# Performance work log

Hardware: AMD Instinct MI355X
Metric: run time of the kernel (lower is better)

Reference implementation:

```python
import jax, jax.numpy as jnp
import numpy as np

EMBED_DIM = 1024
NUM_HEADS = 16
HEAD_DIM = EMBED_DIM // NUM_HEADS
FF_DIM = 4096
B, T, S = 2, 2048, 2048
LN_EPS = 1e-5


def setup_inputs() -> dict:
    key = jax.random.key(0)
    ks = jax.random.split(key, 20)
    sd = 1.0 / np.sqrt(EMBED_DIM)
    d = {
        'x': jax.random.normal(ks[0], (B, T, EMBED_DIM), jnp.float32),
        'encoder_outputs': jax.random.normal(ks[1], (B, S, EMBED_DIM), jnp.float32),
        'tgt_mask': jnp.tril(jnp.ones((T, T), bool))[None, None],  # [1,1,T,T] causal
    }
    # weights stored [in, out] so y = x @ W + b
    names = ['sa_wq', 'sa_wk', 'sa_wv', 'sa_wo', 'ca_wq', 'ca_wk', 'ca_wv', 'ca_wo']
    for i, n in enumerate(names):
        d[n] = jax.random.normal(ks[2 + i], (EMBED_DIM, EMBED_DIM), jnp.float32) * sd
        d[n.replace('w', 'b')] = jnp.zeros((EMBED_DIM,), jnp.float32)
    d['ff_w1'] = jax.random.normal(ks[10], (EMBED_DIM, FF_DIM), jnp.float32) * sd
    d['ff_b1'] = jnp.zeros((FF_DIM,), jnp.float32)
    d['ff_w2'] = jax.random.normal(ks[11], (FF_DIM, EMBED_DIM), jnp.float32) * (1.0 / np.sqrt(FF_DIM))
    d['ff_b2'] = jnp.zeros((EMBED_DIM,), jnp.float32)
    for i in (1, 2, 3):
        d[f'ln{i}_g'] = jnp.ones((EMBED_DIM,), jnp.float32)
        d[f'ln{i}_b'] = jnp.zeros((EMBED_DIM,), jnp.float32)
    return d


def _layernorm(x, g, b):
    mu = jnp.mean(x, -1, keepdims=True)
    var = jnp.mean(jnp.square(x - mu), -1, keepdims=True)
    return (x - mu) * jax.lax.rsqrt(var + LN_EPS) * g + b


def _mha(q_in, k_in, v_in, wq, bq, wk, bk, wv, bv, wo, bo, mask=None):
    Bq, Tq, C = q_in.shape
    Tk = k_in.shape[1]
    Q = (q_in @ wq + bq).reshape(Bq, Tq, NUM_HEADS, HEAD_DIM)
    K = (k_in @ wk + bk).reshape(Bq, Tk, NUM_HEADS, HEAD_DIM)
    V = (v_in @ wv + bv).reshape(Bq, Tk, NUM_HEADS, HEAD_DIM)
    scores = jnp.einsum('bqhd,bkhd->bhqk', Q, K) / np.sqrt(HEAD_DIM)
    if mask is not None:
        scores = jnp.where(mask, scores, -jnp.inf)
    attn = jax.nn.softmax(scores, axis=-1)
    out = jnp.einsum('bhqk,bkhd->bqhd', attn, V).reshape(Bq, Tq, C)
    return out @ wo + bo


def reference(x, encoder_outputs, tgt_mask,
              sa_wq, sa_bq, sa_wk, sa_bk, sa_wv, sa_bv, sa_wo, sa_bo,
              ca_wq, ca_bq, ca_wk, ca_bk, ca_wv, ca_bv, ca_wo, ca_bo,
              ff_w1, ff_b1, ff_w2, ff_b2,
              ln1_g, ln1_b, ln2_g, ln2_b, ln3_g, ln3_b):
    h = _layernorm(x, ln1_g, ln1_b)
    x = x + _mha(h, h, h, sa_wq, sa_bq, sa_wk, sa_bk, sa_wv, sa_bv, sa_wo, sa_bo, tgt_mask)
    h = _layernorm(x, ln2_g, ln2_b)
    x = x + _mha(h, encoder_outputs, encoder_outputs,
                 ca_wq, ca_bq, ca_wk, ca_bk, ca_wv, ca_bv, ca_wo, ca_bo, None)
    h = _layernorm(x, ln3_g, ln3_b)
    ff = jax.nn.relu(h @ ff_w1 + ff_b1) @ ff_w2 + ff_b2
    return x + ff
```

## Files before the change

### kernel.cpp

```cpp
#include <hip/hip_runtime.h>
#include <stdint.h>


typedef __bf16 bf16x8 __attribute__((ext_vector_type(8)));
typedef float  f32x4  __attribute__((ext_vector_type(4)));

#define T_SEQ 2048
#define NROWS 4096
#define QSCALE 0.18033688011112042f

__device__ __forceinline__ unsigned short f2bf(float f) {
  union { float f; unsigned int u; } v; v.f = f;
  unsigned int u = v.u;
  return (unsigned short)((u + 0x7FFFu + ((u >> 16) & 1u)) >> 16);
}
__device__ __forceinline__ float bf2f(unsigned short h) {
  union { unsigned int u; float f; } v; v.u = ((unsigned int)h) << 16;
  return v.f;
}
__device__ __forceinline__ unsigned int pk2(float a, float b) {
  return (unsigned int)f2bf(a) | ((unsigned int)f2bf(b) << 16);
}
__device__ __forceinline__ unsigned int pk2t(float a, float b) {
  union { float f; unsigned int u; } ua, ub;
  ua.f = a; ub.f = b;
  return __builtin_amdgcn_perm(ub.u, ua.u, 0x07060302u);
}
__device__ __forceinline__ float fexp2(float x) {
  return __builtin_amdgcn_exp2f(x);
}
union U4 { unsigned int u[4]; bf16x8 v; };

__global__ void probe_dtype_kernel(const unsigned short* __restrict__ p,
                                   int* __restrict__ flag) {
  __shared__ int cnt;
  if (threadIdx.x == 0) cnt = 0;
  __syncthreads();
  int bad = 0;
  for (int i = threadIdx.x; i < 4096; i += 256) {
    unsigned short u = p[i];
    int e = (u >> 7) & 0xFF;
    if (u != 0 && (e < 100 || e > 140)) bad++;
  }
  atomicAdd(&cnt, bad);
  __syncthreads();
  if (threadIdx.x == 0) *flag = (cnt < 512) ? 1 : 0;
}

struct WTbl {
  const void* src[10];
  int K[10], N[10], start[10];
  unsigned int dstoff[10];
};
__global__ void wtrans_fused_kernel(WTbl tbl, unsigned short* __restrict__ wsbase,
                                    const int* __restrict__ flag) {
  __shared__ unsigned short tile[32][33];
  const int lb = blockIdx.x;
  int wi = 0;
#pragma unroll
  for (int i = 1; i < 10; i++) wi = (lb >= tbl.start[i]) ? i : wi;
  const int local = lb - tbl.start[wi];
  const int Nw = tbl.N[wi], Kw = tbl.K[wi];
  const int bx = local & ((Nw >> 5) - 1);
  const int by = local / (Nw >> 5);
  const void* W = tbl.src[wi];
  unsigned short* Wt = wsbase + tbl.dstoff[wi];
  const int n0 = bx * 32, k0 = by * 32;
  const int c = threadIdx.x & 31, r0 = threadIdx.x >> 5;
  const bool isbf = (*flag != 0);
  for (int r = r0; r < 32; r += 8) {
    unsigned short v;
    if (isbf) v = ((const unsigned short*)W)[(size_t)(k0 + r) * Nw + n0 + c];
    else      v = f2bf(((const float*)W)[(size_t)(k0 + r) * Nw + n0 + c]);
    tile[r][c] = v;
  }
  __syncthreads();
  for (int r = r0; r < 32; r += 8)
    Wt[(size_t)(n0 + r) * Kw + k0 + c] = tile[c][r];
}

struct PTbl { const void* p[19]; };
__global__ void param_cvt_kernel(PTbl tbl, float* __restrict__ out,
                                 const int* __restrict__ flag) {
  const int blk = blockIdx.x;
  const int off = (blk >= 8 && blk < 12) ? (blk - 8) * 1024 : 0;
  const void* src = tbl.p[blk];
  const int i = threadIdx.x * 4;
  float4 o;
  if (*flag) {
    const unsigned short* u = (const unsigned short*)src + off;
    ushort4 q = *(const ushort4*)&u[i];
    o.x = bf2f(q.x); o.y = bf2f(q.y); o.z = bf2f(q.z); o.w = bf2f(q.w);
  } else {
    o = *(const float4*)&((const float*)src)[off + i];
  }
  *(float4*)&out[blk * 1024 + i] = o;
}

__global__ void cvt_to_bf16_kernel(const void* __restrict__ in,
                                   unsigned short* __restrict__ out,
                                   int n, const int* __restrict__ flag) {
  int i = (blockIdx.x * 256 + threadIdx.x) * 8;
  if (i >= n) return;
  if (*flag) {
    *(int4*)&out[i] = *(const int4*)&((const unsigned short*)in)[i];
  } else {
    const float* f = (const float*)in;
    float4 a = *(const float4*)&f[i];
    float4 c = *(const float4*)&f[i + 4];
    ushort4 o1, o2;
    o1.x = f2bf(a.x); o1.y = f2bf(a.y); o1.z = f2bf(a.z); o1.w = f2bf(a.w);
    o2.x = f2bf(c.x); o2.y = f2bf(c.y); o2.z = f2bf(c.z); o2.w = f2bf(c.w);
    *(ushort4*)&out[i] = o1;
    *(ushort4*)&out[i + 4] = o2;
  }
}

__global__ void cvt_to_f32_kernel(const void* __restrict__ in,
                                  float* __restrict__ out,
                                  int n, const int* __restrict__ flag) {
  int i = (blockIdx.x * 256 + threadIdx.x) * 4;
  if (i >= n) return;
  if (*flag) {
    const unsigned short* u = (const unsigned short*)in;
    ushort4 q = *(const ushort4*)&u[i];
    float4 o;
    o.x = bf2f(q.x); o.y = bf2f(q.y); o.z = bf2f(q.z); o.w = bf2f(q.w);
    *(float4*)&out[i] = o;
  } else {
    *(float4*)&out[i] = *(const float4*)&((const float*)in)[i];
  }
}

__global__ __launch_bounds__(256) void ln_kernel(
    const float* __restrict__ x, const float* __restrict__ g,
    const float* __restrict__ b, unsigned short* __restrict__ out) {
  const int row = blockIdx.x;
  const int t = threadIdx.x;
  const size_t base = (size_t)row * 1024;
  float4 v = *(const float4*)&x[base + t * 4];
  float s1 = v.x + v.y + v.z + v.w;
  float s2 = v.x * v.x + v.y * v.y + v.z * v.z + v.w * v.w;
#pragma unroll
  for (int d = 1; d < 64; d <<= 1) {
    s1 += __shfl_xor(s1, d, 64);
    s2 += __shfl_xor(s2, d, 64);
  }
  __shared__ float a1[4], a2[4];
  if ((t & 63) == 0) { a1[t >> 6] = s1; a2[t >> 6] = s2; }
  __syncthreads();
  s1 = a1[0] + a1[1] + a1[2] + a1[3];
  s2 = a2[0] + a2[1] + a2[2] + a2[3];
  const float mean = s1 * (1.0f / 1024.0f);
  const float var = s2 * (1.0f / 1024.0f) - mean * mean;
  const float rstd = rsqrtf(fmaxf(var, 0.0f) + 1e-5f);
  float4 gv = *(const float4*)&g[t * 4];
  float4 bv = *(const float4*)&b[t * 4];
  ushort4 o;
  o.x = f2bf((v.x - mean) * rstd * gv.x + bv.x);
  o.y = f2bf((v.y - mean) * rstd * gv.y + bv.y);
  o.z = f2bf((v.z - mean) * rstd * gv.z + bv.z);
  o.w = f2bf((v.w - mean) * rstd * gv.w + bv.w);
  *(ushort4*)&out[base + t * 4] = o;
}

template <int BM, int BN, int BK, int RELU, int RESID, int OUTM, int BIASROW,
          int SCALEMODE>
__global__ __launch_bounds__(256, 2) void gemm_kernel(
    const unsigned short* __restrict__ A, const unsigned short* __restrict__ Bt,
    const float* __restrict__ bias, const float* __restrict__ resid,
    void* __restrict__ outp, int M, int N, int K,
    const int* __restrict__ flag) {
  static_assert(BK == 64, "swizzle assumes 8 chunks/row");
  constexpr int WX = (BN == 64) ? 1 : 2;
  constexpr int WY = 4 / WX;
  constexpr int WM = BM / WY, WN = BN / WX;
  constexpr int MI = WM / 16, NJ = WN / 16;
  constexpr int ACALLS = BM * BK / 2048;
  constexpr int BCALLS = BN * BK / 2048;
  constexpr int RPC = 2048 / BK;
  __shared__ unsigned short lsA[2][BM * BK];
  __shared__ unsigned short lsB[2][BN * BK];
  const int t = threadIdx.x;
  const int wave = t >> 6, lane = t & 63;
  const int ml = lane & 15, quad = lane >> 4;
  const int cx = ml & 7;
  const int wm = (wave / WX) * WM, wn = (wave % WX) * WN;

  const int nx = gridDim.x, ny = gridDim.y;
  const int lin = (int)blockIdx.y * nx + (int)blockIdx.x;
  const int per = 8 * nx;
  const int y0 = (lin / per) * 8;
  const int gsz = (ny - y0 < 8) ? (ny - y0) : 8;
  const int by = y0 + (lin % gsz);
  const int bx = (lin % per) / gsz;
  const size_t m0 = (size_t)by * BM;
  const size_t n0 = (size_t)bx * BN;

  f32x4 acc[MI][NJ];
  const f32x4 fz = {0.f, 0.f, 0.f, 0.f};
#pragma unroll
  for (int i = 0; i < MI; i++)
#pragma unroll
    for (int j = 0; j < NJ; j++) acc[i][j] = fz;

  const int rowL = t >> 3;
  const int colL = (((t & 7) ^ ((t >> 3) & 7)) * 8);
  const unsigned short* gA = A + (m0 + rowL) * (size_t)K + colL;
  const unsigned short* gB = Bt + (n0 + rowL) * (size_t)K + colL;

  auto stage = [&](int buf, int k0) {
#pragma unroll
    for (int c = 0; c < ACALLS; c++)
      __builtin_amdgcn_global_load_lds(
          (const __attribute__((address_space(1))) void*)(gA + (size_t)(c * RPC) * K + k0),
          (__attribute__((address_space(3))) void*)&lsA[buf][c * 2048 + wave * 512], 16, 0, 0);
#pragma unroll
    for (int c = 0; c < BCALLS; c++)
      __builtin_amdgcn_global_load_lds(
          (const __attribute__((address_space(1))) void*)(gB + (size_t)(c * RPC) * K + k0),
          (__attribute__((address_space(3))) void*)&lsB[buf][c * 2048 + wave * 512], 16, 0, 0);
  };

  stage(0, 0);
  const int nk = K / BK;
  for (int tk = 0; tk < nk; ++tk) {
    const int cur = tk & 1;
    asm volatile("s_waitcnt vmcnt(0)" ::: "memory");
    __builtin_amdgcn_s_barrier();
    if (tk + 1 < nk) stage(cur ^ 1, (tk + 1) * BK);
#pragma unroll
    for (int h = 0; h < BK / 32; h++) {
      bf16x8 af[MI], bfv[NJ];
#pragma unroll
      for (int i = 0; i < MI; i++)
        af[i] = *(const bf16x8*)
            &lsA[cur][(wm + i * 16 + ml) * BK + (((h * 4 + quad) ^ cx) * 8)];
#pragma unroll
      for (int j = 0; j < NJ; j++)
        bfv[j] = *(const bf16x8*)
            &lsB[cur][(wn + j * 16 + ml) * BK + (((h * 4 + quad) ^ cx) * 8)];
#pragma unroll
      for (int i = 0; i < MI; i++)
#pragma unroll
        for (int j = 0; j < NJ; j++)
          acc[i][j] = __builtin_amdgcn_mfma_f32_16x16x32_bf16(af[i], bfv[j],
                                                              acc[i][j], 0, 0, 0);
    }
  }

  const bool obf = (OUTM == 1) || (OUTM == 2 && *flag != 0);
#pragma unroll
  for (int j = 0; j < NJ; j++) {
    const size_t cg = n0 + wn + j * 16 + ml;
    const float bcol = BIASROW ? 0.0f : bias[cg];
    const float sc = (SCALEMODE == 0) ? 1.0f
                   : (SCALEMODE == 1) ? QSCALE
                                      : (cg < 1024 ? QSCALE : 1.0f);
#pragma unroll
    for (int i = 0; i < MI; i++) {
#pragma unroll
      for (int r = 0; r < 4; r++) {
        const size_t rg = m0 + wm + i * 16 + quad * 4 + r;
        const float bval = BIASROW ? bias[rg] : bcol;
        float v = (acc[i][j][r] + bval) * sc;
        if (RELU) v = fmaxf(v, 0.0f);
        if (RESID) v += resid[rg * N + cg];
        if (obf) ((unsigned short*)outp)[rg * N + cg] = f2bf(v);
        else     ((float*)outp)[rg * N + cg] = v;
      }
    }
  }
}

struct GSeg {
  const unsigned short* A; const unsigned short* B;
  const float* bias; unsigned short* out;
  int N, K, start, gxlog2, mode;
};
template <int NSEG>
__global__ __launch_bounds__(256, 4) void gemm_multi_kernel(GSeg s0, GSeg s1,
                                                            GSeg s2) {
  constexpr int BM = 128, BN = 64, BK = 64;
  constexpr int WM = 32, WN = 64;
  constexpr int MI = 2, NJ = 4;
  __shared__ unsigned short lsA[BM * BK];
  __shared__ unsigned short lsB[BN * BK];
  const int blk = (int)blockIdx.x;
  GSeg sg = s0;
  if (NSEG > 1 && blk >= s1.start) sg = s1;
  if (NSEG > 2 && blk >= s2.start) sg = s2;
  const int t = threadIdx.x;
  const int wave = t >> 6, lane = t & 63;
  const int ml = lane & 15, quad = lane >> 4;
  const int cx = ml & 7;
  const int wm = wave * WM, wn = 0;
  const int N = sg.N, K = sg.K;

  const int lin = blk - sg.start;
  const int per = 8 << sg.gxlog2;
  const int y0 = (lin / per) * 8;
  const int by = y0 + (lin & 7);
  const int bx = (lin & (per - 1)) >> 3;
  const size_t m0 = (size_t)by * BM;
  const size_t n0 = (size_t)bx * BN;

  f32x4 acc[MI][NJ];
  const f32x4 fz = {0.f, 0.f, 0.f, 0.f};
#pragma unroll
  for (int i = 0; i < MI; i++)
#pragma unroll
    for (int j = 0; j < NJ; j++) acc[i][j] = fz;

  const int rowL = t >> 3;
  const int colL = (((t & 7) ^ ((t >> 3) & 7)) * 8);
  const unsigned short* gA = sg.A + (m0 + rowL) * (size_t)K + colL;
  const unsigned short* gB = sg.B + (n0 + rowL) * (size_t)K + colL;

  for (int k0 = 0; k0 < K; k0 += BK) {
    __syncthreads();
#pragma unroll
    for (int c = 0; c < 4; c++)
      __builtin_amdgcn_global_load_lds(
          (const __attribute__((address_space(1))) void*)(gA + (size_t)(c * 32) * K + k0),
          (__attribute__((address_space(3))) void*)&lsA[c * 2048 + wave * 512], 16, 0, 0);
#pragma unroll
    for (int c = 0; c < 2; c++)
      __builtin_amdgcn_global_load_lds(
          (const __attribute__((address_space(1))) void*)(gB + (size_t)(c * 32) * K + k0),
          (__attribute__((address_space(3))) void*)&lsB[c * 2048 + wave * 512], 16, 0, 0);
    __syncthreads();
#pragma unroll
    for (int h = 0; h < BK / 32; h++) {
      bf16x8 af[MI], bfv[NJ];
#pragma unroll
      for (int i = 0; i < MI; i++)
        af[i] = *(const bf16x8*)
            &lsA[(wm + i * 16 + ml) * BK + (((h * 4 + quad) ^ cx) * 8)];
#pragma unroll
      for (int j = 0; j < NJ; j++)
        bfv[j] = *(const bf16x8*)
            &lsB[(wn + j * 16 + ml) * BK + (((h * 4 + quad) ^ cx) * 8)];
#pragma unroll
      for (int i = 0; i < MI; i++)
#pragma unroll
        for (int j = 0; j < NJ; j++)
          acc[i][j] = __builtin_amdgcn_mfma_f32_16x16x32_bf16(af[i], bfv[j],
                                                              acc[i][j], 0, 0, 0);
    }
  }

  const int mode = sg.mode;
#pragma unroll
  for (int j = 0; j < NJ; j++) {
    const size_t cg = n0 + wn + j * 16 + ml;
    const float bcol = (mode & 1) ? 0.0f : sg.bias[cg];
    const float sc = (mode & 2) ? QSCALE
                   : ((mode & 4) && cg < 1024) ? QSCALE : 1.0f;
#pragma unroll
    for (int i = 0; i < MI; i++) {
#pragma unroll
      for (int r = 0; r < 4; r++) {
        const size_t rg = m0 + wm + i * 16 + quad * 4 + r;
        const float bval = (mode & 1) ? sg.bias[rg] : bcol;
        float v = (acc[i][j][r] + bval) * sc;
        sg.out[rg * N + cg] = f2bf(v);
      }
    }
  }
}

template <int CAUSAL>
__global__ __launch_bounds__(256, 4) void attn_kernel(
    const unsigned short* __restrict__ Q, const unsigned short* __restrict__ K,
    const unsigned short* __restrict__ VT, unsigned short* __restrict__ O,
    int qstride, int kstride) {
  __shared__ unsigned short Ks[4096];
  __shared__ unsigned short Vs[4096];
  __shared__ unsigned short Qs[4608];
  const int t = threadIdx.x;
  const int wave = t >> 6, lane = t & 63;
  const int ml = lane & 15, quad = lane >> 4;
  const int cx = ml & 7;
  const int bh = blockIdx.y, b = bh >> 4, h = bh & 15;
  const int qb = CAUSAL ? ((int)gridDim.x - 1 - (int)blockIdx.x) : (int)blockIdx.x;
  const int q0 = qb * 64;
  const int lr = lane >> 3;
  const int scol = (((lane & 7) ^ lr) * 8);

  {
    const unsigned short* g0 =
        Q + ((size_t)(b * T_SEQ + q0 + wave * 16 + lr)) * qstride + h * 64 + scol;
    __builtin_amdgcn_global_load_lds(
        (const __attribute__((address_space(1))) void*)g0,
        (__attribute__((address_space(3))) void*)&Qs[wave * 2 * 512], 16, 0, 0);
    const unsigned short* g1 = g0 + (size_t)8 * qstride;
    __builtin_amdgcn_global_load_lds(
        (const __attribute__((address_space(1))) void*)g1,
        (__attribute__((address_space(3))) void*)&Qs[(wave * 2 + 1) * 512], 16, 0, 0);
  }

  int sp_[2];
#pragma unroll
  for (int i = 0; i < 2; i++) {
    int p = (wave * 2 + i) * 8 + lr;
    sp_[i] = ((p & 16) << 1) | ((p & 12) << 1) | ((p & 32) >> 3) | (p & 3);
  }
  const unsigned short* kg0 =
      K + ((size_t)b * T_SEQ + sp_[0]) * kstride + h * 64 + scol;
  const unsigned short* kg1 =
      K + ((size_t)b * T_SEQ + sp_[1]) * kstride + h * 64 + scol;
  const unsigned short* vg0 =
      VT + ((size_t)(h * 64 + wave * 16 + lr)) * 4096 + (size_t)b * T_SEQ + scol;
  const unsigned short* vg1 = vg0 + (size_t)8 * 4096;

  __syncthreads();
  const bf16x8 aq0 = *(const bf16x8*)&Qs[(wave * 16 + ml) * 64 + ((quad ^ cx) * 8)];
  const bf16x8 aq1 = *(const bf16x8*)&Qs[(wave * 16 + ml) * 64 + (((quad + 4) ^ cx) * 8)];

  f32x4 acc[4];
  const f32x4 fz = {0.f, 0.f, 0.f, 0.f};
#pragma unroll
  for (int n = 0; n < 4; n++) acc[n] = fz;
  float m_i = -3.0e38f, l_part = 0.0f;
  const int q_glob = q0 + wave * 16 + ml;
  const int nkb = CAUSAL ? (qb + 1) : (T_SEQ / 64);
  const size_t kinc = (size_t)64 * kstride;

  for (int kb = 0; kb < nkb; kb++) {
    __syncthreads();
    __builtin_amdgcn_global_load_lds(
        (const __attribute__((address_space(1))) void*)kg0,
        (__attribute__((address_space(3))) void*)&Ks[(wave * 2) * 512], 16, 0, 0);
    __builtin_amdgcn_global_load_lds(
        (const __attribute__((address_space(1))) void*)kg1,
        (__attribute__((address_space(3))) void*)&Ks[(wave * 2 + 1) * 512], 16, 0, 0);
    __builtin_amdgcn_global_load_lds(
        (const __attribute__((address_space(1))) void*)vg0,
        (__attribute__((address_space(3))) void*)&Vs[(wave * 2) * 512], 16, 0, 0);
    __builtin_amdgcn_global_load_lds(
        (const __attribute__((address_space(1))) void*)vg1,
        (__attribute__((address_space(3))) void*)&Vs[(wave * 2 + 1) * 512], 16, 0, 0);
    kg0 += kinc; kg1 += kinc; vg0 += 64; vg1 += 64;
    __syncthreads();

    f32x4 s[4];
#pragma unroll
    for (int nt = 0; nt < 4; nt++) {
      bf16x8 k0 = *(const bf16x8*)&Ks[(nt * 16 + ml) * 64 + ((quad ^ cx) * 8)];
      bf16x8 k1 = *(const bf16x8*)&Ks[(nt * 16 + ml) * 64 + (((quad + 4) ^ cx) * 8)];
      f32x4 a = fz;
      a = __builtin_amdgcn_mfma_f32_16x16x32_bf16(k0, aq0, a, 0, 0, 0);
      a = __builtin_amdgcn_mfma_f32_16x16x32_bf16(k1, aq1, a, 0, 0, 0);
      s[nt] = a;
    }
    if (CAUSAL && kb == nkb - 1) {
#pragma unroll
      for (int nt = 0; nt < 4; nt++)
#pragma unroll
        for (int r = 0; r < 4; r++) {
          int key = kb * 64 + ((nt & 1) << 5) + (quad << 3) + ((nt >> 1) << 2) + r;
          if (key > q_glob) s[nt][r] = -3.0e38f;
        }
    }
    float tm = -3.0e38f;
#pragma unroll
    for (int nt = 0; nt < 4; nt++)
#pragma unroll
      for (int r = 0; r < 4; r++) tm = fmaxf(tm, s[nt][r]);
    tm = fmaxf(tm, __shfl_xor(tm, 16));
    tm = fmaxf(tm, __shfl_xor(tm, 32));
    if (__any(tm > m_i)) {
      const float m_new = fmaxf(m_i, tm);
      const float alpha = fexp2(m_i - m_new);
      l_part *= alpha;
#pragma unroll
      for (int n = 0; n < 4; n++)
#pragma unroll
        for (int r = 0; r < 4; r++) acc[n][r] *= alpha;
      m_i = m_new;
    }
    float p[4][4];
    float rs = 0.f;
#pragma unroll
    for (int nt = 0; nt < 4; nt++)
#pragma unroll
      for (int r = 0; r < 4; r++) {
        p[nt][r] = fexp2(s[nt][r] - m_i);
        rs += p[nt][r];
      }
    l_part += rs;

    U4 P0, P1;
    P0.u[0] = pk2t(p[0][0], p[0][1]); P0.u[1] = pk2t(p[0][2], p[0][3]);
    P0.u[2] = pk2t(p[2][0], p[2][1]); P0.u[3] = pk2t(p[2][2], p[2][3]);
    P1.u[0] = pk2t(p[1][0], p[1][1]); P1.u[1] = pk2t(p[1][2], p[1][3]);
    P1.u[2] = pk2t(p[3][0], p[3][1]); P1.u[3] = pk2t(p[3][2], p[3][3]);

#pragma unroll
    for (int n = 0; n < 4; n++) {
      bf16x8 v0 = *(const bf16x8*)&Vs[(n * 16 + ml) * 64 + ((quad ^ cx) * 8)];
      bf16x8 v1 = *(const bf16x8*)&Vs[(n * 16 + ml) * 64 + (((quad + 4) ^ cx) * 8)];
      acc[n] = __builtin_amdgcn_mfma_f32_16x16x32_bf16(v0, P0.v, acc[n], 0, 0, 0);
      acc[n] = __builtin_amdgcn_mfma_f32_16x16x32_bf16(v1, P1.v, acc[n], 0, 0, 0);
    }
  }

  float l_i = l_part;
  l_i += __shfl_xor(l_i, 16);
  l_i += __shfl_xor(l_i, 32);

  const float inv = 1.0f / l_i;
#pragma unroll
  for (int n = 0; n < 4; n++)
#pragma unroll
    for (int rp = 0; rp < 2; rp++) {
      unsigned int u = pk2(acc[n][2 * rp] * inv, acc[n][2 * rp + 1] * inv);
      *(unsigned int*)&Qs[(wave * 16 + ml) * 72 + n * 16 + quad * 4 + 2 * rp] = u;
    }
  __syncthreads();
  {
    const int q = t >> 2, d0 = (t & 3) * 16;
    unsigned short* og = O + ((size_t)(b * T_SEQ + q0 + q)) * 1024 + h * 64 + d0;
    *(int4*)og = *(const int4*)&Qs[q * 72 + d0];
    *(int4*)(og + 8) = *(const int4*)&Qs[q * 72 + d0 + 8];
  }
}

extern "C" void kernel_launch(void* const* d_in, const int* in_sizes, int n_in,
                              void* d_out, int out_size, void* d_ws,
                              size_t ws_size, hipStream_t stream) {
  (void)in_sizes; (void)n_in; (void)out_size; (void)ws_size;
  const size_t MEG = 1048576;
  unsigned short* ws16 = (unsigned short*)d_ws;
  char* wsb = (char*)d_ws;

  unsigned short* wt[10];
  for (int i = 0; i < 8; i++) wt[i] = ws16 + (size_t)i * MEG;
  wt[8] = ws16 + 8 * MEG;
  wt[9] = ws16 + 12 * MEG;
  unsigned short* encB  = ws16 + 16 * MEG;
  unsigned short* hbuf  = ws16 + 20 * MEG;
  unsigned short* QKb   = ws16 + 24 * MEG;
  unsigned short* Qb    = ws16 + 32 * MEG;
  unsigned short* Kb    = ws16 + 36 * MEG;
  unsigned short* Vb    = ws16 + 40 * MEG;
  unsigned short* attnb = ws16 + 44 * MEG;
  unsigned short* ffh   = ws16 + 24 * MEG;
  float* xf32 = (float*)(wsb + 96 * MEG);
  float* pbuf = (float*)(wsb + 112 * MEG);
  int* flag   = (int*)(wsb + 113 * MEG);

  probe_dtype_kernel<<<1, 256, 0, stream>>>((const unsigned short*)d_in[0], flag);

  {
    WTbl tb;
    const int widx[10] = {3, 5, 7, 9, 11, 13, 15, 17, 19, 21};
    int st = 0;
    for (int i = 0; i < 10; i++) {
      tb.src[i] = d_in[widx[i]];
      tb.K[i] = (i == 9) ? 4096 : 1024;
      tb.N[i] = (i == 8) ? 4096 : 1024;
      tb.start[i] = st;
      st += (tb.K[i] / 32) * (tb.N[i] / 32);
      tb.dstoff[i] = (unsigned int)((i < 8) ? i * MEG : (i == 8 ? 8 * MEG : 12 * MEG));
    }
    wtrans_fused_kernel<<<16384, 256, 0, stream>>>(tb, ws16, flag);
  }

  cvt_to_f32_kernel<<<4096, 256, 0, stream>>>(d_in[0], xf32, 4194304, flag);
  cvt_to_bf16_kernel<<<2048, 256, 0, stream>>>(d_in[1], encB, 4194304, flag);

  {
    PTbl pt;
    const int pidx[19] = {4, 6, 8, 10, 12, 14, 16, 18,
                          20, 20, 20, 20, 22, 23, 24, 25, 26, 27, 28};
    for (int i = 0; i < 19; i++) pt.p[i] = d_in[pidx[i]];
    param_cvt_kernel<<<19, 256, 0, stream>>>(pt, pbuf, flag);
  }
  float* bqk_sa = pbuf;
  float* bv_sa  = pbuf + 2048;
  float* bo_sa  = pbuf + 3072;
  float* bq_ca  = pbuf + 4096;
  float* bk_ca  = pbuf + 5120;
  float* bv_ca  = pbuf + 6144;
  float* bo_ca  = pbuf + 7168;
  float* ff_b1p = pbuf + 8192;
  float* ff_b2p = pbuf + 12288;
  float* ln1g = pbuf + 13312; float* ln1b = pbuf + 14336;
  float* ln2g = pbuf + 15360; float* ln2b = pbuf + 16384;
  float* ln3g = pbuf + 17408; float* ln3b = pbuf + 18432;

  dim3 gP(16, 32);
  dim3 gFF1(32, 32);
  dim3 gFF2(8, 64);
  dim3 gAttn(32, 32);

  ln_kernel<<<4096, 256, 0, stream>>>(xf32, ln1g, ln1b, hbuf);
  {
    GSeg sQK = {hbuf, wt[0], bqk_sa, QKb, 2048, 1024, 0, 5, 4};
    GSeg sVT = {wt[2], hbuf, bv_sa, Vb, 4096, 1024, 1024, 6, 1};
    gemm_multi_kernel<2><<<1536, 256, 0, stream>>>(sQK, sVT, sVT);
  }
  attn_kernel<1><<<gAttn, 256, 0, stream>>>(QKb, QKb + 1024, Vb, attnb, 2048, 2048);
  gemm_kernel<128, 64, 64, 0, 1, 0, 0, 0><<<gP, 256, 0, stream>>>(
      attnb, wt[3], bo_sa, xf32, xf32, NROWS, 1024, 1024, nullptr);

  ln_kernel<<<4096, 256, 0, stream>>>(xf32, ln2g, ln2b, hbuf);
  {
    GSeg sQ = {hbuf, wt[4], bq_ca, Qb, 1024, 1024, 0, 4, 2};
    GSeg sK = {encB, wt[5], bk_ca, Kb, 1024, 1024, 512, 4, 0};
    GSeg sV = {wt[6], encB, bv_ca, Vb, 4096, 1024, 1024, 6, 1};
    gemm_multi_kernel<3><<<1536, 256, 0, stream>>>(sQ, sK, sV);
  }
  attn_kernel<0><<<gAttn, 256, 0, stream>>>(Qb, Kb, Vb, attnb, 1024, 1024);
  gemm_kernel<128, 64, 64, 0, 1, 0, 0, 0><<<gP, 256, 0, stream>>>(
      attnb, wt[7], bo_ca, xf32, xf32, NROWS, 1024, 1024, nullptr);

  ln_kernel<<<4096, 256, 0, stream>>>(xf32, ln3g, ln3b, hbuf);
  gemm_kernel<128, 128, 64, 1, 0, 1, 0, 0><<<gFF1, 256, 0, stream>>>(
      hbuf, wt[8], ff_b1p, nullptr, ffh, NROWS, 4096, 1024, nullptr);
  gemm_kernel<64, 128, 64, 0, 1, 2, 0, 0><<<gFF2, 256, 0, stream>>>(
      ffh, wt[9], ff_b2p, xf32, d_out, NROWS, 1024, 4096, flag);
}
```

Baseline: 587.5 us.

## Add triple-buffered LDS pipeline to output-projection and FF2 GEMMs

```diff
diff --git a/kernel.cpp b/kernel.cpp
--- a/kernel.cpp
+++ b/kernel.cpp
@@ -30,6 +30,13 @@
   return __builtin_amdgcn_exp2f(x);
 }
 union U4 { unsigned int u[4]; bf16x8 v; };
+
+template <int N> __device__ __forceinline__ void wait_vm() {
+  static_assert(N == 0 || N == 6 || N == 8, "add string for this N");
+  if constexpr (N == 0) asm volatile("s_waitcnt vmcnt(0)" ::: "memory");
+  if constexpr (N == 6) asm volatile("s_waitcnt vmcnt(6)" ::: "memory");
+  if constexpr (N == 8) asm volatile("s_waitcnt vmcnt(8)" ::: "memory");
+}
 
 __global__ void probe_dtype_kernel(const unsigned short* __restrict__ p,
                                    int* __restrict__ flag) {
@@ -164,8 +171,8 @@
   *(ushort4*)&out[base + t * 4] = o;
 }
 
-template <int BM, int BN, int BK, int RELU, int RESID, int OUTM, int BIASROW,
-          int SCALEMODE>
+template <int BM, int BN, int BK, int D, int RELU, int RESID, int OUTM,
+          int BIASROW, int SCALEMODE>
 __global__ __launch_bounds__(256, 2) void gemm_kernel(
     const unsigned short* __restrict__ A, const unsigned short* __restrict__ Bt,
     const float* __restrict__ bias, const float* __restrict__ resid,
@@ -179,8 +186,9 @@
   constexpr int ACALLS = BM * BK / 2048;
   constexpr int BCALLS = BN * BK / 2048;
   constexpr int RPC = 2048 / BK;
-  __shared__ unsigned short lsA[2][BM * BK];
-  __shared__ unsigned short lsB[2][BN * BK];
+  constexpr int S = ACALLS + BCALLS;
+  __shared__ unsigned short lsA[D][BM * BK];
+  __shared__ unsigned short lsB[D][BN * BK];
   const int t = threadIdx.x;
   const int wave = t >> 6, lane = t & 63;
   const int ml = lane & 15, quad = lane >> 4;
@@ -209,43 +217,86 @@
   const unsigned short* gA = A + (m0 + rowL) * (size_t)K + colL;
   const unsigned short* gB = Bt + (n0 + rowL) * (size_t)K + colL;
 
-  auto stage = [&](int buf, int k0) {
+  auto stage = [&](unsigned short* dA, unsigned short* dB, int k0) {
 #pragma unroll
     for (int c = 0; c < ACALLS; c++)
       __builtin_amdgcn_global_load_lds(
           (const __attribute__((address_space(1))) void*)(gA + (size_t)(c * RPC) * K + k0),
-          (__attribute__((address_space(3))) void*)&lsA[buf][c * 2048 + wave * 512], 16, 0, 0);
+          (__attribute__((address_space(3))) void*)(dA + c * 2048 + wave * 512), 16, 0, 0);
 #pragma unroll
     for (int c = 0; c < BCALLS; c++)
       __builtin_amdgcn_global_load_lds(
           (const __attribute__((address_space(1))) void*)(gB + (size_t)(c * RPC) * K + k0),
-          (__attribute__((address_space(3))) void*)&lsB[buf][c * 2048 + wave * 512], 16, 0, 0);
+          (__attribute__((address_space(3))) void*)(dB + c * 2048 + wave * 512), 16, 0, 0);
   };
-
-  stage(0, 0);
-  const int nk = K / BK;
-  for (int tk = 0; tk < nk; ++tk) {
-    const int cur = tk & 1;
-    asm volatile("s_waitcnt vmcnt(0)" ::: "memory");
-    __builtin_amdgcn_s_barrier();
-    if (tk + 1 < nk) stage(cur ^ 1, (tk + 1) * BK);
+  auto comp = [&](const unsigned short* bA, const unsigned short* bB) {
 #pragma unroll
     for (int h = 0; h < BK / 32; h++) {
       bf16x8 af[MI], bfv[NJ];
 #pragma unroll
       for (int i = 0; i < MI; i++)
         af[i] = *(const bf16x8*)
-            &lsA[cur][(wm + i * 16 + ml) * BK + (((h * 4 + quad) ^ cx) * 8)];
+            &bA[(wm + i * 16 + ml) * BK + (((h * 4 + quad) ^ cx) * 8)];
 #pragma unroll
       for (int j = 0; j < NJ; j++)
         bfv[j] = *(const bf16x8*)
-            &lsB[cur][(wn + j * 16 + ml) * BK + (((h * 4 + quad) ^ cx) * 8)];
+            &bB[(wn + j * 16 + ml) * BK + (((h * 4 + quad) ^ cx) * 8)];
 #pragma unroll
       for (int i = 0; i < MI; i++)
 #pragma unroll
         for (int j = 0; j < NJ; j++)
           acc[i][j] = __builtin_amdgcn_mfma_f32_16x16x32_bf16(af[i], bfv[j],
                                                               acc[i][j], 0, 0, 0);
+    }
+  };
+
+  const int nk = K / BK;
+  stage(lsA[0], lsB[0], 0);
+  if constexpr (D == 3) {
+    stage(lsA[1], lsB[1], BK);
+    int tb = 0;
+    while (tb + 3 <= nk) {
+      wait_vm<S>();
+      __builtin_amdgcn_s_barrier();
+      stage(lsA[2], lsB[2], (tb + 2) * BK);
+      comp(lsA[0], lsB[0]);
+      wait_vm<S>();
+      __builtin_amdgcn_s_barrier();
+      if (tb + 3 < nk) stage(lsA[0], lsB[0], (tb + 3) * BK);
+      comp(lsA[1], lsB[1]);
+      if (tb + 3 < nk) wait_vm<S>(); else wait_vm<0>();
+      __builtin_amdgcn_s_barrier();
+      if (tb + 4 < nk) stage(lsA[1], lsB[1], (tb + 4) * BK);
+      comp(lsA[2], lsB[2]);
+      tb += 3;
+    }
+    const int r = nk - tb;
+    if (r == 1) {
+      wait_vm<0>();
+      __builtin_amdgcn_s_barrier();
+      comp(lsA[0], lsB[0]);
+    } else if (r == 2) {
+      wait_vm<S>();
+      __builtin_amdgcn_s_barrier();
+      comp(lsA[0], lsB[0]);
+      wait_vm<0>();
+      __builtin_amdgcn_s_barrier();
+      comp(lsA[1], lsB[1]);
+    }
+  } else {
+    int tk = 0;
+    while (tk < nk) {
+      wait_vm<0>();
+      __builtin_amdgcn_s_barrier();
+      if (tk + 1 < nk) stage(lsA[1], lsB[1], (tk + 1) * BK);
+      comp(lsA[0], lsB[0]);
+      if (tk + 1 < nk) {
+        wait_vm<0>();
+        __builtin_amdgcn_s_barrier();
+        if (tk + 2 < nk) stage(lsA[0], lsB[0], (tk + 2) * BK);
+        comp(lsA[1], lsB[1]);
+      }
+      tk += 2;
     }
   }
 
@@ -603,7 +654,7 @@
     gemm_multi_kernel<2><<<1536, 256, 0, stream>>>(sQK, sVT, sVT);
   }
   attn_kernel<1><<<gAttn, 256, 0, stream>>>(QKb, QKb + 1024, Vb, attnb, 2048, 2048);
-  gemm_kernel<128, 64, 64, 0, 1, 0, 0, 0><<<gP, 256, 0, stream>>>(
+  gemm_kernel<128, 64, 64, 3, 0, 1, 0, 0, 0><<<gP, 256, 0, stream>>>(
       attnb, wt[3], bo_sa, xf32, xf32, NROWS, 1024, 1024, nullptr);
 
   ln_kernel<<<4096, 256, 0, stream>>>(xf32, ln2g, ln2b, hbuf);
@@ -614,12 +665,12 @@
     gemm_multi_kernel<3><<<1536, 256, 0, stream>>>(sQ, sK, sV);
   }
   attn_kernel<0><<<gAttn, 256, 0, stream>>>(Qb, Kb, Vb, attnb, 1024, 1024);
-  gemm_kernel<128, 64, 64, 0, 1, 0, 0, 0><<<gP, 256, 0, stream>>>(
+  gemm_kernel<128, 64, 64, 3, 0, 1, 0, 0, 0><<<gP, 256, 0, stream>>>(
       attnb, wt[7], bo_ca, xf32, xf32, NROWS, 1024, 1024, nullptr);
 
   ln_kernel<<<4096, 256, 0, stream>>>(xf32, ln3g, ln3b, hbuf);
-  gemm_kernel<128, 128, 64, 1, 0, 1, 0, 0><<<gFF1, 256, 0, stream>>>(
+  gemm_kernel<128, 128, 64, 2, 1, 0, 1, 0, 0><<<gFF1, 256, 0, stream>>>(
       hbuf, wt[8], ff_b1p, nullptr, ffh, NROWS, 4096, 1024, nullptr);
-  gemm_kernel<64, 128, 64, 0, 1, 2, 0, 0><<<gFF2, 256, 0, stream>>>(
+  gemm_kernel<64, 128, 64, 3, 0, 1, 2, 0, 0><<<gFF2, 256, 0, stream>>>(
       ffh, wt[9], ff_b2p, xf32, d_out, NROWS, 1024, 4096, flag);
 }
```

After: 572.5 us. 2.5% less time.

## Prepack weights into MFMA fragment layout and load B directly to registers

Applied to the files above, without the earlier changes.

```diff
diff --git a/kernel.cpp b/kernel.cpp
--- a/kernel.cpp
+++ b/kernel.cpp
@@ -75,8 +75,19 @@
     tile[r][c] = v;
   }
   __syncthreads();
-  for (int r = r0; r < 32; r += 8)
-    Wt[(size_t)(n0 + r) * Kw + k0 + c] = tile[c][r];
+  const bool packed = (wi == 3) || (wi >= 7);
+  if (!packed) {
+    for (int r = r0; r < 32; r += 8)
+      Wt[(size_t)(n0 + r) * Kw + k0 + c] = tile[c][r];
+  } else {
+    const int k = k0 + c;
+    const size_t kpart = ((size_t)(k >> 5) << 9) + ((((k >> 3) & 3) << 7) + (k & 7));
+    const size_t kfr = (size_t)(Kw >> 5);
+    for (int r = r0; r < 32; r += 8) {
+      const int n = n0 + r;
+      Wt[((size_t)(n >> 4) * kfr << 9) + kpart + ((n & 15) << 3)] = tile[c][r];
+    }
+  }
 }
 
 struct PTbl { const void* p[19]; };
@@ -164,8 +175,8 @@
   *(ushort4*)&out[base + t * 4] = o;
 }
 
-template <int BM, int BN, int BK, int RELU, int RESID, int OUTM, int BIASROW,
-          int SCALEMODE>
+template <int BM, int BN, int BK, int RELU, int RESID, int OUTM,
+          int BIASROW, int SCALEMODE>
 __global__ __launch_bounds__(256, 2) void gemm_kernel(
     const unsigned short* __restrict__ A, const unsigned short* __restrict__ Bt,
     const float* __restrict__ bias, const float* __restrict__ resid,
@@ -177,10 +188,8 @@
   constexpr int WM = BM / WY, WN = BN / WX;
   constexpr int MI = WM / 16, NJ = WN / 16;
   constexpr int ACALLS = BM * BK / 2048;
-  constexpr int BCALLS = BN * BK / 2048;
   constexpr int RPC = 2048 / BK;
   __shared__ unsigned short lsA[2][BM * BK];
-  __shared__ unsigned short lsB[2][BN * BK];
   const int t = threadIdx.x;
   const int wave = t >> 6, lane = t & 63;
   const int ml = lane & 15, quad = lane >> 4;
@@ -207,46 +216,58 @@
   const int rowL = t >> 3;
   const int colL = (((t & 7) ^ ((t >> 3) & 7)) * 8);
   const unsigned short* gA = A + (m0 + rowL) * (size_t)K + colL;
-  const unsigned short* gB = Bt + (n0 + rowL) * (size_t)K + colL;
-
-  auto stage = [&](int buf, int k0) {
+  const int kfr = K >> 5;
+  const unsigned short* gBp =
+      Bt + ((size_t)((n0 + wn) >> 4) * kfr) * 512 + lane * 8;
+
+  auto stageA = [&](unsigned short* dA, int k0) {
 #pragma unroll
     for (int c = 0; c < ACALLS; c++)
       __builtin_amdgcn_global_load_lds(
           (const __attribute__((address_space(1))) void*)(gA + (size_t)(c * RPC) * K + k0),
-          (__attribute__((address_space(3))) void*)&lsA[buf][c * 2048 + wave * 512], 16, 0, 0);
-#pragma unroll
-    for (int c = 0; c < BCALLS; c++)
-      __builtin_amdgcn_global_load_lds(
-          (const __attribute__((address_space(1))) void*)(gB + (size_t)(c * RPC) * K + k0),
-          (__attribute__((address_space(3))) void*)&lsB[buf][c * 2048 + wave * 512], 16, 0, 0);
+          (__attribute__((address_space(3))) void*)(dA + c * 2048 + wave * 512), 16, 0, 0);
   };
-
-  stage(0, 0);
+  auto loadB = [&](bf16x8 (&bq)[NJ][2], int k0) {
+#pragma unroll
+    for (int j = 0; j < NJ; j++)
+#pragma unroll
+      for (int h = 0; h < 2; h++)
+        bq[j][h] = *(const bf16x8*)(gBp + ((size_t)j * kfr + (k0 >> 5) + h) * 512);
+  };
+  auto comp = [&](const unsigned short* bA, const bf16x8 (&bq)[NJ][2]) {
+#pragma unroll
+    for (int h = 0; h < 2; h++) {
+      bf16x8 af[MI];
+#pragma unroll
+      for (int i = 0; i < MI; i++)
+        af[i] = *(const bf16x8*)
+            &bA[(wm + i * 16 + ml) * BK + (((h * 4 + quad) ^ cx) * 8)];
+#pragma unroll
+      for (int i = 0; i < MI; i++)
+#pragma unroll
+        for (int j = 0; j < NJ; j++)
+          acc[i][j] = __builtin_amdgcn_mfma_f32_16x16x32_bf16(af[i], bq[j][h],
+                                                              acc[i][j], 0, 0, 0);
+    }
+  };
+
   const int nk = K / BK;
-  for (int tk = 0; tk < nk; ++tk) {
-    const int cur = tk & 1;
+  bf16x8 bq0[NJ][2], bq1[NJ][2];
+  stageA(&lsA[0][0], 0);
+  loadB(bq0, 0);
+  int tk = 0;
+  while (tk < nk) {
     asm volatile("s_waitcnt vmcnt(0)" ::: "memory");
     __builtin_amdgcn_s_barrier();
-    if (tk + 1 < nk) stage(cur ^ 1, (tk + 1) * BK);
-#pragma unroll
-    for (int h = 0; h < BK / 32; h++) {
-      bf16x8 af[MI], bfv[NJ];
-#pragma unroll
-      for (int i = 0; i < MI; i++)
-        af[i] = *(const bf16x8*)
-            &lsA[cur][(wm + i * 16 + ml) * BK + (((h * 4 + quad) ^ cx) * 8)];
-#pragma unroll
-      for (int j = 0; j < NJ; j++)
-        bfv[j] = *(const bf16x8*)
-            &lsB[cur][(wn + j * 16 + ml) * BK + (((h * 4 + quad) ^ cx) * 8)];
-#pragma unroll
-      for (int i = 0; i < MI; i++)
-#pragma unroll
-        for (int j = 0; j < NJ; j++)
-          acc[i][j] = __builtin_amdgcn_mfma_f32_16x16x32_bf16(af[i], bfv[j],
-                                                              acc[i][j], 0, 0, 0);
-    }
+    if (tk + 1 < nk) { stageA(&lsA[1][0], (tk + 1) * BK); loadB(bq1, (tk + 1) * BK); }
+    comp(&lsA[0][0], bq0);
+    if (tk + 1 < nk) {
+      asm volatile("s_waitcnt vmcnt(0)" ::: "memory");
+      __builtin_amdgcn_s_barrier();
+      if (tk + 2 < nk) { stageA(&lsA[0][0], (tk + 2) * BK); loadB(bq0, (tk + 2) * BK); }
+      comp(&lsA[1][0], bq1);
+    }
+    tk += 2;
   }
 
   const bool obf = (OUTM == 1) || (OUTM == 2 && *flag != 0);
```

After: 577.3 us. No clear change (-1.7%).
